# Optimization experiments

Measured on AMD Instinct MI355X. Metric: run time of the kernel, lower is better.

## Reference

```python
import jax, jax.numpy as jnp
import numpy as np

D_MODEL = 1024
N_HEAD = 16
D_HEAD = D_MODEL // N_HEAD


def setup_inputs() -> dict:
    key = jax.random.key(0)
    k_x, k_wqkv, k_bqkv, k_wp, k_bp = jax.random.split(key, 5)
    B, T = 2, 2048
    bound = 1.0 / np.sqrt(D_MODEL)
    return {
        "x": jax.random.normal(k_x, (B, T, D_MODEL), dtype=jnp.float32),
        "w_qkv": jax.random.uniform(k_wqkv, (D_MODEL, 3 * D_MODEL), jnp.float32, -bound, bound),
        "b_qkv": jax.random.uniform(k_bqkv, (3 * D_MODEL,), jnp.float32, -bound, bound),
        "w_proj": jax.random.uniform(k_wp, (D_MODEL, D_MODEL), jnp.float32, -bound, bound),
        "b_proj": jax.random.uniform(k_bp, (D_MODEL,), jnp.float32, -bound, bound),
    }


def reference(x, w_qkv, b_qkv, w_proj, b_proj):
    B, T, C = x.shape
    qkv = x @ w_qkv + b_qkv                       # [B,T,3C]
    qkv = qkv.reshape(B, T, 3, N_HEAD, D_HEAD)
    qkv = jnp.transpose(qkv, (2, 0, 3, 1, 4))      # [3,B,H,T,dh]
    q, k, v = qkv[0], qkv[1], qkv[2]
    scale = np.sqrt(D_HEAD).astype(np.float32)
    attn = jnp.einsum("bhqd,bhkd->bhqk", q, k) / scale  # [B,H,T,T]
    causal = jnp.tril(jnp.ones((T, T), dtype=bool))
    attn = jnp.where(causal, attn, -jnp.inf)
    attn = jax.nn.softmax(attn, axis=-1)
    out = jnp.einsum("bhqk,bhkd->bhqd", attn, v)   # [B,H,T,dh]
    out = jnp.transpose(out, (0, 2, 1, 3)).reshape(B, T, C)
    return out @ w_proj + b_proj
```

## Files before the change

kernel.cpp:

```cpp
#include <hip/hip_runtime.h>
#include <hip/hip_bf16.h>
#include <math.h>

constexpr int Bb   = 2;
constexpr int T    = 2048;
constexpr int C    = 1024;
constexpr int H    = 16;
constexpr int M    = Bb * T;
constexpr int NQKV = 3 * C;

typedef __attribute__((ext_vector_type(8))) short bf16x8;
typedef __attribute__((ext_vector_type(4))) float f32x4;
typedef __attribute__((ext_vector_type(16))) float f32x16;

__device__ inline short f2bf(float f) {
    __hip_bfloat16 h = __float2bfloat16(f);
    return *reinterpret_cast<short*>(&h);
}

#if __has_builtin(__builtin_amdgcn_exp2f)
#define EXP2(x) __builtin_amdgcn_exp2f(x)
#else
#define EXP2(x) exp2f(x)
#endif

#define GLOBAL_AS __attribute__((address_space(1)))
#define LDS_AS    __attribute__((address_space(3)))

__device__ __forceinline__ void gload_lds16(const short* g, short* s) {
    __builtin_amdgcn_global_load_lds((const GLOBAL_AS void*)g, (LDS_AS void*)s, 16, 0, 0);
}

__global__ __launch_bounds__(256)
void prep_all(const float* __restrict__ x, short* __restrict__ xb,
              const float* __restrict__ w_qkv, short* __restrict__ wqkvt,
              const float* __restrict__ w_proj, short* __restrict__ wprojt)
{
    __shared__ float tile[32][33];
    const int blk = blockIdx.x;
    const int tid = threadIdx.x;

    if (blk < 4096) {
        const int i = blk * 1024 + tid * 4;
        const float4 v = *(const float4*)(x + i);
        short4 s;
        s.x = f2bf(v.x); s.y = f2bf(v.y); s.z = f2bf(v.z); s.w = f2bf(v.w);
        *(short4*)(xb + i) = s;
        return;
    }

    const bool isqkv = (blk < 7168);
    const int bidx = isqkv ? (blk - 4096) : (blk - 7168);
    const int nblk = isqkv ? 96 : 32;
    const int N    = isqkv ? NQKV : C;
    const float* W = isqkv ? w_qkv : w_proj;
    short* Wt      = isqkv ? wqkvt : wprojt;

    const int n0 = (bidx % nblk) * 32, k0 = (bidx / nblk) * 32;
    const int tx = tid & 31, ty = tid >> 5;
#pragma unroll
    for (int i = 0; i < 32; i += 8)
        tile[ty + i][tx] = W[(size_t)(k0 + ty + i) * N + n0 + tx];
    __syncthreads();
#pragma unroll
    for (int i = 0; i < 32; i += 8)
        Wt[(size_t)(n0 + ty + i) * C + k0 + tx] = f2bf(tile[tx][ty + i]);
}

__global__ __launch_bounds__(256)
void gemm_mfma(const short* __restrict__ A, const short* __restrict__ Bt,
               const float* __restrict__ bias, short* __restrict__ outp,
               int Ndim, int Kdim)
{
    __shared__ __align__(16) short As[2 * 128 * 32];
    __shared__ __align__(16) short Bs[2 * 128 * 32];

    const int tid = threadIdx.x;
    const int w   = tid >> 6;
    const int l   = tid & 63;
    const int lk  = l & 15;
    const int lq  = l >> 4;

    const int gx  = gridDim.x;
    const int nwg = gx * gridDim.y;
    const int cpx = nwg >> 3;
    const int bid = blockIdx.y * gx + blockIdx.x;
    const int swz = (bid & 7) * cpx + (bid >> 3);
    const int m0  = (swz / gx) * 128;
    const int n0  = (swz % gx) * 128;

    const int mw  = (w >> 1) * 64, nw = (w & 1) * 64;

    const int srow = w * 16 + (l >> 2);
    const int scol = (l & 3) * 8;

    const short* agp0 = A  + (size_t)(m0 + srow)      * Kdim + scol;
    const short* agp1 = A  + (size_t)(m0 + 64 + srow) * Kdim + scol;
    const short* bgp0 = Bt + (size_t)(n0 + srow)      * Kdim + scol;
    const short* bgp1 = Bt + (size_t)(n0 + 64 + srow) * Kdim + scol;

    short* ad0 = &As[w * 512];
    short* ad1 = &As[2048 + w * 512];
    short* bd0 = &Bs[w * 512];
    short* bd1 = &Bs[2048 + w * 512];

    f32x4 acc[4][4];
#pragma unroll
    for (int i = 0; i < 4; ++i)
#pragma unroll
        for (int j = 0; j < 4; ++j) acc[i][j] = (f32x4){0.f, 0.f, 0.f, 0.f};

    gload_lds16(agp0, ad0);
    gload_lds16(agp1, ad1);
    gload_lds16(bgp0, bd0);
    gload_lds16(bgp1, bd1);
    __syncthreads();

    int cur = 0;
    for (int k0 = 0; k0 < Kdim; k0 += 32) {
        const int coff = cur ? 4096 : 0;

        bf16x8 af[4], bfr[4];
#pragma unroll
        for (int mt = 0; mt < 4; ++mt)
            af[mt] = *(const bf16x8*)&As[coff + (mw + mt * 16 + lk) * 32 + lq * 8];
#pragma unroll
        for (int nt = 0; nt < 4; ++nt)
            bfr[nt] = *(const bf16x8*)&Bs[coff + (nw + nt * 16 + lk) * 32 + lq * 8];

        if (k0 + 32 < Kdim) {
            const int noff = cur ? 0 : 4096;
            gload_lds16(agp0 + k0 + 32, ad0 + noff);
            gload_lds16(agp1 + k0 + 32, ad1 + noff);
            gload_lds16(bgp0 + k0 + 32, bd0 + noff);
            gload_lds16(bgp1 + k0 + 32, bd1 + noff);
        }

#pragma unroll
        for (int mt = 0; mt < 4; ++mt)
#pragma unroll
            for (int nt = 0; nt < 4; ++nt)
                acc[mt][nt] = __builtin_amdgcn_mfma_f32_16x16x32_bf16(bfr[nt], af[mt], acc[mt][nt], 0, 0, 0);

        __syncthreads();
        cur ^= 1;
    }

    float4 bv[4];
#pragma unroll
    for (int nt = 0; nt < 4; ++nt)
        bv[nt] = *(const float4*)(bias + n0 + nw + nt * 16 + lq * 4);
#pragma unroll
    for (int mt = 0; mt < 4; ++mt) {
        short* rowp = outp + (size_t)(m0 + mw + mt * 16 + lk) * Ndim + n0 + nw + lq * 4;
#pragma unroll
        for (int nt = 0; nt < 4; ++nt) {
            short4 pk;
            pk.x = f2bf(acc[mt][nt][0] + bv[nt].x);
            pk.y = f2bf(acc[mt][nt][1] + bv[nt].y);
            pk.z = f2bf(acc[mt][nt][2] + bv[nt].z);
            pk.w = f2bf(acc[mt][nt][3] + bv[nt].w);
            *(short4*)(rowp + nt * 16) = pk;
        }
    }
}

__global__ __launch_bounds__(256)
void gemm_mfma_proj(const short* __restrict__ A, const short* __restrict__ Bt,
                    const float* __restrict__ bias, float* __restrict__ outp,
                    int Ndim, int Kdim)
{
    __shared__ __align__(16) short As[2 * 64 * 32];
    __shared__ __align__(16) short Bs[2 * 128 * 32];

    const int tid = threadIdx.x;
    const int w   = tid >> 6;
    const int l   = tid & 63;
    const int lk  = l & 15;
    const int lq  = l >> 4;

    const int gx  = gridDim.x;
    const int nwg = gx * gridDim.y;
    const int cpx = nwg >> 3;
    const int bid = blockIdx.y * gx + blockIdx.x;
    const int swz = (bid & 7) * cpx + (bid >> 3);
    const int m0  = (swz / gx) * 64;
    const int n0  = (swz % gx) * 128;

    const int mw  = (w & 1) * 32, nw = (w >> 1) * 64;

    const int srow = w * 16 + (l >> 2);
    const int scol = (l & 3) * 8;

    const short* agp  = A  + (size_t)(m0 + srow)      * Kdim + scol;
    const short* bgp0 = Bt + (size_t)(n0 + srow)      * Kdim + scol;
    const short* bgp1 = Bt + (size_t)(n0 + 64 + srow) * Kdim + scol;

    short* ad  = &As[w * 512];
    short* bd0 = &Bs[w * 512];
    short* bd1 = &Bs[2048 + w * 512];

    f32x4 acc[2][4];
#pragma unroll
    for (int i = 0; i < 2; ++i)
#pragma unroll
        for (int j = 0; j < 4; ++j) acc[i][j] = (f32x4){0.f, 0.f, 0.f, 0.f};

    gload_lds16(agp,  ad);
    gload_lds16(bgp0, bd0);
    gload_lds16(bgp1, bd1);
    __syncthreads();

    int cur = 0;
    for (int k0 = 0; k0 < Kdim; k0 += 32) {
        const int coffA = cur ? 2048 : 0;
        const int coffB = cur ? 4096 : 0;

        bf16x8 af[2], bfr[4];
#pragma unroll
        for (int mt = 0; mt < 2; ++mt)
            af[mt] = *(const bf16x8*)&As[coffA + (mw + mt * 16 + lk) * 32 + lq * 8];
#pragma unroll
        for (int nt = 0; nt < 4; ++nt)
            bfr[nt] = *(const bf16x8*)&Bs[coffB + (nw + nt * 16 + lk) * 32 + lq * 8];

        if (k0 + 32 < Kdim) {
            const int noffA = cur ? 0 : 2048;
            const int noffB = cur ? 0 : 4096;
            gload_lds16(agp  + k0 + 32, ad  + noffA);
            gload_lds16(bgp0 + k0 + 32, bd0 + noffB);
            gload_lds16(bgp1 + k0 + 32, bd1 + noffB);
        }

#pragma unroll
        for (int mt = 0; mt < 2; ++mt)
#pragma unroll
            for (int nt = 0; nt < 4; ++nt)
                acc[mt][nt] = __builtin_amdgcn_mfma_f32_16x16x32_bf16(bfr[nt], af[mt], acc[mt][nt], 0, 0, 0);

        __syncthreads();
        cur ^= 1;
    }

    float4 bv[4];
#pragma unroll
    for (int nt = 0; nt < 4; ++nt)
        bv[nt] = *(const float4*)(bias + n0 + nw + nt * 16 + lq * 4);
#pragma unroll
    for (int mt = 0; mt < 2; ++mt) {
        float* rowp = outp + (size_t)(m0 + mw + mt * 16 + lk) * Ndim + n0 + nw + lq * 4;
#pragma unroll
        for (int nt = 0; nt < 4; ++nt) {
            float4 v;
            v.x = acc[mt][nt][0] + bv[nt].x;
            v.y = acc[mt][nt][1] + bv[nt].y;
            v.z = acc[mt][nt][2] + bv[nt].z;
            v.w = acc[mt][nt][3] + bv[nt].w;
            *(float4*)(rowp + nt * 16) = v;
        }
    }
}

constexpr float SC = 0.18033688f;
constexpr float M0 = 16.0f;

__global__ __launch_bounds__(256, 2)
void attn_mfma(const short* __restrict__ qkv, short* __restrict__ att)
{
    __shared__ __align__(16) short Ks[2][128 * 64];
    __shared__ __align__(16) short Vt[2][64 * 128];

    const int idx = blockIdx.x;
    const int xcd = idx & 7;
    const int j   = idx >> 3;
    const int bh  = xcd * 4 + (j & 3);
    const int s   = j >> 2;
    const int qt  = (s < 8) ? s : (23 - s);
    const int b   = bh >> 4;
    const int h   = bh & 15;
    const int qbase = qt * 128;
    const int nkt   = qt + 1;

    const int tid = threadIdx.x;
    const int w   = tid >> 6;
    const int l   = tid & 63;
    const int c31 = l & 31;
    const int hi  = l >> 5;

    const short* base = qkv + (size_t)b * T * 3072 + h * 64;

    const int q_abs = qbase + w * 32 + c31;
    const short* qp = base + (size_t)q_abs * 3072 + hi * 8;
    bf16x8 qf[4];
#pragma unroll
    for (int ds = 0; ds < 4; ++ds)
        qf[ds] = *(const bf16x8*)(qp + ds * 16);

    f32x16 acc_o[2];
#pragma unroll
    for (int dt = 0; dt < 2; ++dt)
#pragma unroll
        for (int r = 0; r < 16; ++r) acc_o[dt][r] = 0.f;
    float lacc = 0.f;

    const int kswz = 8 * ((l & 7) ^ (l >> 3));
    const int sw   = c31 & 7;

    const int k0v = 2 * l;
    const int kk5 = k0v & 31;
    const int pos = (k0v >> 5) * 32 + ((kk5 >> 4) & 1) * 16 + ((kk5 >> 2) & 1) * 8
                  + ((kk5 >> 3) & 1) * 4 + (kk5 & 3);
    const int vg  = pos >> 3;
    const int vpo = pos & 7;
    const int seg = w * 16;
    const int dmask = c31 & 15;

    union { uint4 q[2]; unsigned int u[8]; } KA, KB;

#pragma unroll
    for (int rr = 0; rr < 4; ++rr) {
        const int rowbase = rr * 32 + w * 8;
        gload_lds16(base + 1024 + (size_t)(rowbase + (l >> 3)) * 3072 + kswz,
                    &Ks[0][rowbase * 64]);
    }
    {
        const short* vp = base + 2048 + (size_t)k0v * 3072 + seg;
        KA.q[0] = *(const uint4*)vp;
        KA.q[1] = *(const uint4*)(vp + 8);
        KB.q[0] = *(const uint4*)(vp + 3072);
        KB.q[1] = *(const uint4*)(vp + 3080);
#pragma unroll
        for (int dd = 0; dd < 16; ++dd) {
            const unsigned int w0 = KA.u[dd >> 1];
            const unsigned int w1 = KB.u[dd >> 1];
            const unsigned int pk = (dd & 1) ? ((w0 >> 16) | (w1 & 0xffff0000u))
                                             : ((w0 & 0xffffu) | (w1 << 16));
            *(unsigned int*)&Vt[0][(seg + dd) * 128 + ((vg ^ dd) << 3) + vpo] = pk;
        }
    }
    __syncthreads();

#pragma unroll 1
    for (int it = 0; it < nkt; ++it) {
        const int j0  = it * 128;
        const int buf = it & 1;
        const int nb  = buf ^ 1;
        const bool diag  = (it == nkt - 1);
        const int  ktmax = diag ? w : 3;

        if (it + 1 < nkt) {
            const int j1 = j0 + 128;
#pragma unroll
            for (int rr = 0; rr < 4; ++rr) {
                const int rowbase = rr * 32 + w * 8;
                gload_lds16(base + 1024 + (size_t)(j1 + rowbase + (l >> 3)) * 3072 + kswz,
                            &Ks[nb][rowbase * 64]);
            }
            const short* vp = base + 2048 + (size_t)(j1 + k0v) * 3072 + seg;
            KA.q[0] = *(const uint4*)vp;
            KA.q[1] = *(const uint4*)(vp + 8);
            KB.q[0] = *(const uint4*)(vp + 3072);
            KB.q[1] = *(const uint4*)(vp + 3080);
        }

        f32x16 s4[4];
        __builtin_amdgcn_s_setprio(1);
#pragma unroll
        for (int kb = 0; kb < 4; ++kb) {
            if (kb <= ktmax) {
                const short* krp = &Ks[buf][(kb * 32 + c31) * 64];
                f32x16 a;
#pragma unroll
                for (int r = 0; r < 16; ++r) a[r] = 0.f;
#pragma unroll
                for (int ds = 0; ds < 4; ++ds) {
                    const bf16x8 kf = *(const bf16x8*)&krp[((ds * 2 + hi) ^ sw) << 3];
                    a = __builtin_amdgcn_mfma_f32_32x32x16_bf16(kf, qf[ds], a, 0, 0, 0);
                }
                s4[kb] = a;
            }
        }
        __builtin_amdgcn_s_setprio(0);

        if (diag) {
#pragma unroll
            for (int kb = 0; kb < 4; ++kb) {
                if (kb == ktmax) {
#pragma unroll
                    for (int r = 0; r < 16; ++r) {
                        const int crow = (r & 3) + 8 * (r >> 2) + 4 * hi;
                        if (crow > c31) s4[kb][r] = -1e30f;
                    }
                }
            }
        }

#pragma unroll
        for (int kb = 0; kb < 4; ++kb) {
            if (kb <= ktmax) {
#pragma unroll
                for (int r = 0; r < 16; ++r)
                    s4[kb][r] = EXP2(fmaf(s4[kb][r], SC, -M0));
            }
        }

        float ps = 0.f;
#pragma unroll
        for (int kb = 0; kb < 4; ++kb) {
            if (kb <= ktmax) {
                float a0 = (s4[kb][0] + s4[kb][1]) + (s4[kb][2] + s4[kb][3]);
                float a1 = (s4[kb][4] + s4[kb][5]) + (s4[kb][6] + s4[kb][7]);
                float a2 = (s4[kb][8] + s4[kb][9]) + (s4[kb][10] + s4[kb][11]);
                float a3 = (s4[kb][12] + s4[kb][13]) + (s4[kb][14] + s4[kb][15]);
                ps += (a0 + a1) + (a2 + a3);
            }
        }
        lacc += ps;

        __builtin_amdgcn_s_setprio(1);
#pragma unroll
        for (int kb = 0; kb < 4; ++kb) {
            if (kb <= ktmax) {
#pragma unroll
                for (int hh = 0; hh < 2; ++hh) {
                    union { unsigned int u[4]; bf16x8 v; } up;
#pragma unroll
                    for (int p = 0; p < 4; ++p)
                        up.u[p] = (unsigned int)(unsigned short)f2bf(s4[kb][hh * 8 + 2 * p])
                                | ((unsigned int)(unsigned short)f2bf(s4[kb][hh * 8 + 2 * p + 1]) << 16);
                    const int g = kb * 4 + hh * 2 + hi;
#pragma unroll
                    for (int dt = 0; dt < 2; ++dt) {
                        const bf16x8 vf = *(const bf16x8*)
                            &Vt[buf][(dt * 32 + c31) * 128 + ((g ^ dmask) << 3)];
                        acc_o[dt] = __builtin_amdgcn_mfma_f32_32x32x16_bf16(vf, up.v, acc_o[dt], 0, 0, 0);
                    }
                }
            }
        }
        __builtin_amdgcn_s_setprio(0);

        if (it + 1 < nkt) {
#pragma unroll
            for (int dd = 0; dd < 16; ++dd) {
                const unsigned int w0 = KA.u[dd >> 1];
                const unsigned int w1 = KB.u[dd >> 1];
                const unsigned int pk = (dd & 1) ? ((w0 >> 16) | (w1 & 0xffff0000u))
                                                 : ((w0 & 0xffffu) | (w1 << 16));
                *(unsigned int*)&Vt[nb][(seg + dd) * 128 + ((vg ^ dd) << 3) + vpo] = pk;
            }
        }

        __syncthreads();
    }

    const float ls  = lacc + __shfl_xor(lacc, 32);
    const float inv = 1.f / ls;
    short* op = att + ((size_t)(b * T + q_abs)) * 1024 + h * 64;
#pragma unroll
    for (int dt = 0; dt < 2; ++dt)
#pragma unroll
        for (int rg = 0; rg < 4; ++rg) {
            const int d0 = dt * 32 + 8 * rg + 4 * hi;
            short4 pk;
            pk.x = f2bf(acc_o[dt][rg * 4 + 0] * inv);
            pk.y = f2bf(acc_o[dt][rg * 4 + 1] * inv);
            pk.z = f2bf(acc_o[dt][rg * 4 + 2] * inv);
            pk.w = f2bf(acc_o[dt][rg * 4 + 3] * inv);
            *(short4*)(op + d0) = pk;
        }
}

extern "C" void kernel_launch(void* const* d_in, const int* in_sizes, int n_in,
                              void* d_out, int out_size, void* d_ws, size_t ws_size,
                              hipStream_t stream)
{
    const float* x      = (const float*)d_in[0];
    const float* w_qkv  = (const float*)d_in[1];
    const float* b_qkv  = (const float*)d_in[2];
    const float* w_proj = (const float*)d_in[3];
    const float* b_proj = (const float*)d_in[4];
    float* out = (float*)d_out;

    short* xb     = (short*)d_ws;
    short* wqkvt  = xb     + (size_t)M * C;
    short* wprojt = wqkvt  + (size_t)NQKV * C;
    short* qkvb   = wprojt + (size_t)C * C;
    short* attb   = qkvb   + (size_t)M * NQKV;

    prep_all<<<8192, 256, 0, stream>>>(x, xb, w_qkv, wqkvt, w_proj, wprojt);
    gemm_mfma<<<dim3(NQKV / 128, M / 128), 256, 0, stream>>>(xb, wqkvt, b_qkv, qkvb, NQKV, C);
    attn_mfma<<<512, 256, 0, stream>>>(qkvb, attb);
    gemm_mfma_proj<<<dim3(C / 128, M / 64), 256, 0, stream>>>(attb, wprojt, b_proj, out, C, C);
}
```

Baseline: 197.5 us.

## Split attention key blocks across wave pairs with 512-thread blocks and LDS reduction

Doubles the attention block to 8 waves. Each pair of waves shares 32 query rows and each wave handles half of the 128-key tile, with the partial outputs and softmax sums combined through LDS at the end. K loading and V transposing are now done by separate wave groups instead of by every wave. This is meant to raise occupancy and spread the per-tile work more evenly. In exchange it adds a final reduction pass, does redundant masked work on the diagonal tile, and puts more register pressure on 512-thread blocks with two blocks per CU.

Result: faster. 174.7 us (-11.6%).

```diff
diff --git a/kernel.cpp b/kernel.cpp
--- a/kernel.cpp
+++ b/kernel.cpp
@@ -264,7 +264,7 @@
 constexpr float SC = 0.18033688f;
 constexpr float M0 = 16.0f;
 
-__global__ __launch_bounds__(256, 2)
+__global__ __launch_bounds__(512, 2)
 void attn_mfma(const short* __restrict__ qkv, short* __restrict__ att)
 {
     __shared__ __align__(16) short Ks[2][128 * 64];
@@ -282,14 +282,16 @@
     const int nkt   = qt + 1;
 
     const int tid = threadIdx.x;
-    const int w   = tid >> 6;
-    const int l   = tid & 63;
-    const int c31 = l & 31;
-    const int hi  = l >> 5;
+    const int w    = tid >> 6;
+    const int l    = tid & 63;
+    const int c31  = l & 31;
+    const int hi   = l >> 5;
+    const int pair = w >> 1;
+    const int half = w & 1;
 
     const short* base = qkv + (size_t)b * T * 3072 + h * 64;
 
-    const int q_abs = qbase + w * 32 + c31;
+    const int q_abs = qbase + pair * 32 + c31;
     const short* qp = base + (size_t)q_abs * 3072 + hi * 8;
     bf16x8 qf[4];
 #pragma unroll
@@ -303,6 +305,7 @@
         for (int r = 0; r < 16; ++r) acc_o[dt][r] = 0.f;
     float lacc = 0.f;
 
+    const int w4   = w - 4;
     const int kswz = 8 * ((l & 7) ^ (l >> 3));
     const int sw   = c31 & 7;
 
@@ -312,18 +315,19 @@
                   + ((kk5 >> 3) & 1) * 4 + (kk5 & 3);
     const int vg  = pos >> 3;
     const int vpo = pos & 7;
-    const int seg = w * 16;
+    const int seg = (w & 3) * 16;
     const int dmask = c31 & 15;
 
     union { uint4 q[2]; unsigned int u[8]; } KA, KB;
 
-#pragma unroll
-    for (int rr = 0; rr < 4; ++rr) {
-        const int rowbase = rr * 32 + w * 8;
-        gload_lds16(base + 1024 + (size_t)(rowbase + (l >> 3)) * 3072 + kswz,
-                    &Ks[0][rowbase * 64]);
-    }
-    {
+    if (w >= 4) {
+#pragma unroll
+        for (int rr = 0; rr < 4; ++rr) {
+            const int rowbase = rr * 32 + w4 * 8;
+            gload_lds16(base + 1024 + (size_t)(rowbase + (l >> 3)) * 3072 + kswz,
+                        &Ks[0][rowbase * 64]);
+        }
+    } else {
         const short* vp = base + 2048 + (size_t)k0v * 3072 + seg;
         KA.q[0] = *(const uint4*)vp;
         KA.q[1] = *(const uint4*)(vp + 8);
@@ -345,102 +349,90 @@
         const int j0  = it * 128;
         const int buf = it & 1;
         const int nb  = buf ^ 1;
-        const bool diag  = (it == nkt - 1);
-        const int  ktmax = diag ? w : 3;
 
         if (it + 1 < nkt) {
             const int j1 = j0 + 128;
-#pragma unroll
-            for (int rr = 0; rr < 4; ++rr) {
-                const int rowbase = rr * 32 + w * 8;
-                gload_lds16(base + 1024 + (size_t)(j1 + rowbase + (l >> 3)) * 3072 + kswz,
-                            &Ks[nb][rowbase * 64]);
+            if (w >= 4) {
+#pragma unroll
+                for (int rr = 0; rr < 4; ++rr) {
+                    const int rowbase = rr * 32 + w4 * 8;
+                    gload_lds16(base + 1024 + (size_t)(j1 + rowbase + (l >> 3)) * 3072 + kswz,
+                                &Ks[nb][rowbase * 64]);
+                }
+            } else {
+                const short* vp = base + 2048 + (size_t)(j1 + k0v) * 3072 + seg;
+                KA.q[0] = *(const uint4*)vp;
+                KA.q[1] = *(const uint4*)(vp + 8);
+                KB.q[0] = *(const uint4*)(vp + 3072);
+                KB.q[1] = *(const uint4*)(vp + 3080);
             }
-            const short* vp = base + 2048 + (size_t)(j1 + k0v) * 3072 + seg;
-            KA.q[0] = *(const uint4*)vp;
-            KA.q[1] = *(const uint4*)(vp + 8);
-            KB.q[0] = *(const uint4*)(vp + 3072);
-            KB.q[1] = *(const uint4*)(vp + 3080);
-        }
-
-        f32x16 s4[4];
+        }
+
+        f32x16 s4[2];
         __builtin_amdgcn_s_setprio(1);
 #pragma unroll
-        for (int kb = 0; kb < 4; ++kb) {
-            if (kb <= ktmax) {
-                const short* krp = &Ks[buf][(kb * 32 + c31) * 64];
-                f32x16 a;
-#pragma unroll
-                for (int r = 0; r < 16; ++r) a[r] = 0.f;
-#pragma unroll
-                for (int ds = 0; ds < 4; ++ds) {
-                    const bf16x8 kf = *(const bf16x8*)&krp[((ds * 2 + hi) ^ sw) << 3];
-                    a = __builtin_amdgcn_mfma_f32_32x32x16_bf16(kf, qf[ds], a, 0, 0, 0);
+        for (int kb = 0; kb < 2; ++kb) {
+            const int kbase = half * 2 + kb;
+            const short* krp = &Ks[buf][(kbase * 32 + c31) * 64];
+            f32x16 a;
+#pragma unroll
+            for (int r = 0; r < 16; ++r) a[r] = 0.f;
+#pragma unroll
+            for (int ds = 0; ds < 4; ++ds) {
+                const bf16x8 kf = *(const bf16x8*)&krp[((ds * 2 + hi) ^ sw) << 3];
+                a = __builtin_amdgcn_mfma_f32_32x32x16_bf16(kf, qf[ds], a, 0, 0, 0);
+            }
+            s4[kb] = a;
+        }
+        __builtin_amdgcn_s_setprio(0);
+
+        if (it == nkt - 1) {
+#pragma unroll
+            for (int kb = 0; kb < 2; ++kb)
+#pragma unroll
+                for (int r = 0; r < 16; ++r) {
+                    const int key = j0 + (half * 2 + kb) * 32 + (r & 3) + 8 * (r >> 2) + 4 * hi;
+                    if (key > q_abs) s4[kb][r] = -1e30f;
                 }
-                s4[kb] = a;
-            }
-        }
-        __builtin_amdgcn_s_setprio(0);
-
-        if (diag) {
-#pragma unroll
-            for (int kb = 0; kb < 4; ++kb) {
-                if (kb == ktmax) {
-#pragma unroll
-                    for (int r = 0; r < 16; ++r) {
-                        const int crow = (r & 3) + 8 * (r >> 2) + 4 * hi;
-                        if (crow > c31) s4[kb][r] = -1e30f;
-                    }
+        }
+
+#pragma unroll
+        for (int kb = 0; kb < 2; ++kb)
+#pragma unroll
+            for (int r = 0; r < 16; ++r)
+                s4[kb][r] = EXP2(fmaf(s4[kb][r], SC, -M0));
+
+#pragma unroll
+        for (int kb = 0; kb < 2; ++kb) {
+            float a0 = (s4[kb][0] + s4[kb][1]) + (s4[kb][2] + s4[kb][3]);
+            float a1 = (s4[kb][4] + s4[kb][5]) + (s4[kb][6] + s4[kb][7]);
+            float a2 = (s4[kb][8] + s4[kb][9]) + (s4[kb][10] + s4[kb][11]);
+            float a3 = (s4[kb][12] + s4[kb][13]) + (s4[kb][14] + s4[kb][15]);
+            lacc += (a0 + a1) + (a2 + a3);
+        }
+
+        __builtin_amdgcn_s_setprio(1);
+#pragma unroll
+        for (int kb = 0; kb < 2; ++kb) {
+#pragma unroll
+            for (int hh = 0; hh < 2; ++hh) {
+                union { unsigned int u[4]; bf16x8 v; } up;
+#pragma unroll
+                for (int p = 0; p < 4; ++p)
+                    up.u[p] = (unsigned int)(unsigned short)f2bf(s4[kb][hh * 8 + 2 * p])
+                            | ((unsigned int)(unsigned short)f2bf(s4[kb][hh * 8 + 2 * p + 1]) << 16);
+                const int g = (half * 2 + kb) * 4 + hh * 2 + hi;
+#pragma unroll
+                for (int dt = 0; dt < 2; ++dt) {
+                    const bf16x8 vf = *(const bf16x8*)
+                        &Vt[buf][(dt * 32 + c31) * 128 + ((g ^ dmask) << 3)];
+                    acc_o[dt] = __builtin_amdgcn_mfma_f32_32x32x16_bf16(vf, up.v, acc_o[dt], 0, 0, 0);
                 }
             }
         }
-
-#pragma unroll
-        for (int kb = 0; kb < 4; ++kb) {
-            if (kb <= ktmax) {
-#pragma unroll
-                for (int r = 0; r < 16; ++r)
-                    s4[kb][r] = EXP2(fmaf(s4[kb][r], SC, -M0));
-            }
-        }
-
-        float ps = 0.f;
-#pragma unroll
-        for (int kb = 0; kb < 4; ++kb) {
-            if (kb <= ktmax) {
-                float a0 = (s4[kb][0] + s4[kb][1]) + (s4[kb][2] + s4[kb][3]);
-                float a1 = (s4[kb][4] + s4[kb][5]) + (s4[kb][6] + s4[kb][7]);
-                float a2 = (s4[kb][8] + s4[kb][9]) + (s4[kb][10] + s4[kb][11]);
-                float a3 = (s4[kb][12] + s4[kb][13]) + (s4[kb][14] + s4[kb][15]);
-                ps += (a0 + a1) + (a2 + a3);
-            }
-        }
-        lacc += ps;
-
-        __builtin_amdgcn_s_setprio(1);
-#pragma unroll
-        for (int kb = 0; kb < 4; ++kb) {
-            if (kb <= ktmax) {
-#pragma unroll
-                for (int hh = 0; hh < 2; ++hh) {
-                    union { unsigned int u[4]; bf16x8 v; } up;
-#pragma unroll
-                    for (int p = 0; p < 4; ++p)
-                        up.u[p] = (unsigned int)(unsigned short)f2bf(s4[kb][hh * 8 + 2 * p])
-                                | ((unsigned int)(unsigned short)f2bf(s4[kb][hh * 8 + 2 * p + 1]) << 16);
-                    const int g = kb * 4 + hh * 2 + hi;
-#pragma unroll
-                    for (int dt = 0; dt < 2; ++dt) {
-                        const bf16x8 vf = *(const bf16x8*)
-                            &Vt[buf][(dt * 32 + c31) * 128 + ((g ^ dmask) << 3)];
-                        acc_o[dt] = __builtin_amdgcn_mfma_f32_32x32x16_bf16(vf, up.v, acc_o[dt], 0, 0, 0);
-                    }
-                }
-            }
-        }
         __builtin_amdgcn_s_setprio(0);
 
-        if (it + 1 < nkt) {
+        if (it + 1 < nkt && w < 4) {
 #pragma unroll
             for (int dd = 0; dd < 16; ++dd) {
                 const unsigned int w0 = KA.u[dd >> 1];
@@ -454,21 +446,42 @@
         __syncthreads();
     }
 
-    const float ls  = lacc + __shfl_xor(lacc, 32);
-    const float inv = 1.f / ls;
-    short* op = att + ((size_t)(b * T + q_abs)) * 1024 + h * 64;
-#pragma unroll
-    for (int dt = 0; dt < 2; ++dt)
-#pragma unroll
-        for (int rg = 0; rg < 4; ++rg) {
-            const int d0 = dt * 32 + 8 * rg + 4 * hi;
-            short4 pk;
-            pk.x = f2bf(acc_o[dt][rg * 4 + 0] * inv);
-            pk.y = f2bf(acc_o[dt][rg * 4 + 1] * inv);
-            pk.z = f2bf(acc_o[dt][rg * 4 + 2] * inv);
-            pk.w = f2bf(acc_o[dt][rg * 4 + 3] * inv);
-            *(short4*)(op + d0) = pk;
-        }
+    float* accS = (float*)&Ks[0][0];
+    float* lS   = (float*)&Vt[0][0];
+    const int sb  = (pair * 64 + l) * 32;
+    const int sx  = (l & 7) << 2;
+    if (half == 1) {
+#pragma unroll
+        for (int dt = 0; dt < 2; ++dt)
+#pragma unroll
+            for (int r = 0; r < 16; ++r)
+                accS[sb + ((dt * 16 + r) ^ sx)] = acc_o[dt][r];
+        lS[pair * 64 + l] = lacc;
+    }
+    __syncthreads();
+    if (half == 0) {
+#pragma unroll
+        for (int dt = 0; dt < 2; ++dt)
+#pragma unroll
+            for (int r = 0; r < 16; ++r)
+                acc_o[dt][r] += accS[sb + ((dt * 16 + r) ^ sx)];
+        float lt = lacc + lS[pair * 64 + l];
+        const float ls  = lt + __shfl_xor(lt, 32);
+        const float inv = 1.f / ls;
+        short* op = att + ((size_t)(b * T + q_abs)) * 1024 + h * 64;
+#pragma unroll
+        for (int dt = 0; dt < 2; ++dt)
+#pragma unroll
+            for (int rg = 0; rg < 4; ++rg) {
+                const int d0 = dt * 32 + 8 * rg + 4 * hi;
+                short4 pk;
+                pk.x = f2bf(acc_o[dt][rg * 4 + 0] * inv);
+                pk.y = f2bf(acc_o[dt][rg * 4 + 1] * inv);
+                pk.z = f2bf(acc_o[dt][rg * 4 + 2] * inv);
+                pk.w = f2bf(acc_o[dt][rg * 4 + 3] * inv);
+                *(short4*)(op + d0) = pk;
+            }
+    }
 }
 
 extern "C" void kernel_launch(void* const* d_in, const int* in_sizes, int n_in,
@@ -490,6 +503,6 @@
 
     prep_all<<<8192, 256, 0, stream>>>(x, xb, w_qkv, wqkvt, w_proj, wprojt);
     gemm_mfma<<<dim3(NQKV / 128, M / 128), 256, 0, stream>>>(xb, wqkvt, b_qkv, qkvb, NQKV, C);
-    attn_mfma<<<512, 256, 0, stream>>>(qkvb, attb);
+    attn_mfma<<<512, 512, 0, stream>>>(qkvb, attb);
     gemm_mfma_proj<<<dim3(C / 128, M / 64), 256, 0, stream>>>(attb, wprojt, b_proj, out, C, C);
 }
```
